# Optimization experiments

Measured on AMD Instinct MI355X. Metric: run time of the kernel, lower is better.

Reference implementation:

```python
import jax, jax.numpy as jnp
import numpy as np

NUM_BOND_TYPE = 6
NUM_BOND_DIRECTION = 3
N_NODES = 20000
N_EDGES = 320000
HIDDEN = 256
OUT = 256
N_MASK = 2000


def setup_inputs() -> dict:
    key = jax.random.key(0)
    ks = jax.random.split(key, 12)
    x = jax.random.normal(ks[0], (N_NODES, HIDDEN), dtype=jnp.float32)
    edge_index = jax.random.randint(ks[1], (2, N_EDGES), 0, N_NODES, dtype=jnp.int64)
    edge_attr = jax.random.randint(ks[2], (N_EDGES, 2), 0, 3, dtype=jnp.int64)
    mask_node_indices = jax.random.randint(ks[3], (N_MASK,), 0, N_NODES, dtype=jnp.int64)
    # parameters (torch Linear convention: y = x @ W.T + b)
    def xavier(k, shape):
        fan_in, fan_out = shape[1], shape[0]
        lim = float(np.sqrt(6.0 / (fan_in + fan_out)))
        return jax.random.uniform(k, shape, jnp.float32, -lim, lim)
    prelu_a = jnp.asarray(0.25, dtype=jnp.float32)  # torch PReLU default
    W_enc = xavier(ks[4], (HIDDEN, HIDDEN))          # enc_to_dec, no bias
    E1 = xavier(ks[5], (NUM_BOND_TYPE, HIDDEN))
    E2 = xavier(ks[6], (NUM_BOND_DIRECTION, HIDDEN))
    W1 = xavier(ks[7], (2 * HIDDEN, HIDDEN))
    b1 = jnp.zeros((2 * HIDDEN,), jnp.float32)
    W2 = xavier(ks[8], (OUT, 2 * HIDDEN))
    b2 = jnp.zeros((OUT,), jnp.float32)
    return {"x": x, "edge_index": edge_index, "edge_attr": edge_attr,
            "mask_node_indices": mask_node_indices, "prelu_a": prelu_a,
            "W_enc": W_enc, "E1": E1, "E2": E2,
            "W1": W1, "b1": b1, "W2": W2, "b2": b2}


def reference(x, edge_index, edge_attr, mask_node_indices, prelu_a,
              W_enc, E1, E2, W1, b1, W2, b2):
    N = x.shape[0]
    # PReLU -> enc_to_dec linear (no bias) -> zero masked rows
    x = jnp.where(x >= 0, x, prelu_a * x)
    x = x @ W_enc.T
    x = x.at[mask_node_indices].set(0.0)
    # add self loops: (i,i) edges with attr (4, 0)
    loop = jnp.arange(N, dtype=edge_index.dtype)
    ei = jnp.concatenate([edge_index, jnp.stack([loop, loop])], axis=1)  # [2, E+N]
    loop_attr = jnp.concatenate(
        [jnp.full((N, 1), 4, edge_attr.dtype), jnp.zeros((N, 1), edge_attr.dtype)], axis=1)
    ea = jnp.concatenate([edge_attr, loop_attr], axis=0)                 # [E+N, 2]
    edge_emb = E1[ea[:, 0]] + E2[ea[:, 1]]                               # [E+N, D]
    src, dst = ei[0], ei[1]                                              # j -> i
    msg = x[src] + edge_emb                                              # [E+N, D]
    aggr = jax.ops.segment_sum(msg, dst, num_segments=N)                 # [N, D]
    # GIN MLP: Linear -> ReLU -> Linear
    h = jax.nn.relu(aggr @ W1.T + b1)
    return h @ W2.T + b2
```

## Files before the change

### kernel.cpp

```cpp
#include <hip/hip_runtime.h>

#define HIDDEN 256
#define CAP 64

typedef _Float16 h4_t __attribute__((ext_vector_type(4)));
typedef _Float16 h8_t __attribute__((ext_vector_type(8)));
typedef float    f4_t __attribute__((ext_vector_type(4)));

typedef const __attribute__((address_space(1))) void* gbl_ptr_t;
typedef __attribute__((address_space(3))) void*       lds_ptr_t;

__device__ inline f4_t cvt4(h4_t h) {
    f4_t o; o.x = (float)h.x; o.y = (float)h.y; o.z = (float)h.z; o.w = (float)h.w;
    return o;
}

__global__ __launch_bounds__(256) void k_prep(
        const float* __restrict__ x, _Float16* __restrict__ xh,
        const float* __restrict__ prelu_a, int M, int Mpad, int nb_x,
        const int* __restrict__ ei, const int* __restrict__ ea, int E,
        int* __restrict__ cnt, int* __restrict__ csr, int nb_fill,
        const float* __restrict__ W_enc, const float* __restrict__ W1,
        const float* __restrict__ W2, _Float16* __restrict__ Whenc,
        _Float16* __restrict__ Wh1, _Float16* __restrict__ Wh2, int nb_w,
        const int* __restrict__ mask, unsigned char* __restrict__ flags, int NM) {
    int b = blockIdx.x;
    int t = threadIdx.x;
    if (b < nb_x) {
        int base = (b * 256 + t) * 4;
        if (base >= Mpad * HIDDEN) return;
        int row = base >> 8;
        h4_t o;
        if (row < M) {
            float pa = *prelu_a;
            f4_t v = *(const f4_t*)(x + base);
            o.x = (_Float16)(v.x >= 0.f ? v.x : pa * v.x);
            o.y = (_Float16)(v.y >= 0.f ? v.y : pa * v.y);
            o.z = (_Float16)(v.z >= 0.f ? v.z : pa * v.z);
            o.w = (_Float16)(v.w >= 0.f ? v.w : pa * v.w);
        } else {
            o = (h4_t)(_Float16)0.f;
        }
        *(h4_t*)(xh + base) = o;
        return;
    }
    b -= nb_x;
    if (b < nb_fill) {
        int e = b * 256 + t;
        if (e >= E) return;
        int src = ei[e];
        int dst = ei[E + e];
        int combo = ea[2 * e] * 3 + ea[2 * e + 1];
        int slot = atomicAdd(&cnt[dst], 1);
        if (slot < CAP) csr[dst * CAP + slot] = src | (combo << 16);
        return;
    }
    b -= nb_fill;
    if (b < nb_w) {
        const int n0 = HIDDEN * HIDDEN, n1 = 2 * HIDDEN * HIDDEN, n2 = HIDDEN * 2 * HIDDEN;
        int base = (b * 256 + t) * 4;
        const float* s; _Float16* d; int off;
        if (base < n0) { s = W_enc; d = Whenc; off = base; }
        else if (base < n0 + n1) { s = W1; d = Wh1; off = base - n0; }
        else if (base < n0 + n1 + n2) { s = W2; d = Wh2; off = base - n0 - n1; }
        else return;
        f4_t v = *(const f4_t*)(s + off);
        h4_t o; o.x = (_Float16)v.x; o.y = (_Float16)v.y;
        o.z = (_Float16)v.z; o.w = (_Float16)v.w;
        *(h4_t*)(d + off) = o;
        return;
    }
    b -= nb_w;
    {
        int i = b * 256 + t;
        if (i < NM) flags[mask[i]] = 1;
    }
}

__global__ __launch_bounds__(256) void k_aggregate(
        const _Float16* __restrict__ xe,
        const float* __restrict__ E1, const float* __restrict__ E2,
        const int* __restrict__ cnt, const int* __restrict__ csr,
        _Float16* __restrict__ aggr, int N, int Mpad) {
    __shared__ __align__(16) _Float16 e12h[18 * HIDDEN];
    int t = threadIdx.x;
    for (int idx = t; idx < 18 * 64; idx += 256) {
        int combo = idx >> 6, c4 = (idx & 63) * 4;
        int a1 = combo / 3, a2 = combo - a1 * 3;
        f4_t v1 = *(const f4_t*)(E1 + a1 * HIDDEN + c4);
        f4_t v2 = *(const f4_t*)(E2 + a2 * HIDDEN + c4);
        h4_t o;
        o.x = (_Float16)(v1.x + v2.x); o.y = (_Float16)(v1.y + v2.y);
        o.z = (_Float16)(v1.z + v2.z); o.w = (_Float16)(v1.w + v2.w);
        *(h4_t*)(e12h + combo * HIDDEN + c4) = o;
    }
    __syncthreads();
    int node = blockIdx.x * 4 + (t >> 6);
    if (node >= Mpad) return;
    int lane = t & 63;
    int c0 = lane * 4;
    if (node >= N) {
        *(h4_t*)(aggr + (size_t)node * HIDDEN + c0) = (h4_t)(_Float16)0.f;
        return;
    }
    int deg = cnt[node];
    if (deg > CAP) deg = CAP;
    const int* lst = csr + (size_t)node * CAP;
    int pv = (lane < deg) ? lst[lane] : 0;

    h4_t hs = *(const h4_t*)(xe + (size_t)node * HIDDEN + c0);
    h4_t se = *(const h4_t*)(e12h + 12 * HIDDEN + c0);
    f4_t acc = cvt4(hs) + cvt4(se);

    int e = 0;
    for (; e + 7 < deg; e += 8) {
        int p[8]; h4_t hv[8], qv[8];
#pragma unroll
        for (int j = 0; j < 8; ++j) p[j] = __shfl(pv, e + j, 64);
#pragma unroll
        for (int j = 0; j < 8; ++j)
            hv[j] = *(const h4_t*)(xe + (size_t)(p[j] & 0xFFFF) * HIDDEN + c0);
#pragma unroll
        for (int j = 0; j < 8; ++j)
            qv[j] = *(const h4_t*)(e12h + (p[j] >> 16) * HIDDEN + c0);
        h4_t s0 = (hv[0] + qv[0]) + (hv[1] + qv[1]);
        h4_t s1 = (hv[2] + qv[2]) + (hv[3] + qv[3]);
        h4_t s2 = (hv[4] + qv[4]) + (hv[5] + qv[5]);
        h4_t s3 = (hv[6] + qv[6]) + (hv[7] + qv[7]);
        acc += cvt4(s0) + cvt4(s1);
        acc += cvt4(s2) + cvt4(s3);
    }
    for (; e < deg; ++e) {
        int p = __shfl(pv, e, 64);
        h4_t h = *(const h4_t*)(xe + (size_t)(p & 0xFFFF) * HIDDEN + c0);
        h4_t q = *(const h4_t*)(e12h + (p >> 16) * HIDDEN + c0);
        acc += cvt4(h + q);
    }
    h4_t o;
    o.x = (_Float16)acc.x; o.y = (_Float16)acc.y;
    o.z = (_Float16)acc.z; o.w = (_Float16)acc.w;
    *(h4_t*)(aggr + (size_t)node * HIDDEN + c0) = o;
}

template <int K, bool RELU, bool HAS_BIAS, bool OUT_F16, bool MASK>
__global__ __launch_bounds__(256) void k_gemm128(
        const _Float16* __restrict__ A, const _Float16* __restrict__ B,
        const float* __restrict__ bias, void* __restrict__ Cout,
        const unsigned char* __restrict__ flags, int Mstore, int N) {
    __shared__ __align__(16) _Float16 As[128 * 32];
    __shared__ __align__(16) _Float16 Bs[128 * 32];
    int t = threadIdx.x;
    int w = t >> 6, L = t & 63;
    int wr = (w >> 1) * 64, wc = (w & 1) * 64;
    int m0 = blockIdx.y * 128, n0 = blockIdx.x * 128;
    int lr = L & 15, lk = (L >> 4) * 8;

    f4_t acc[4][4] = {};

    auto stage = [&](int k0) {
#pragma unroll
        for (int i = 0; i < 2; ++i) {
            int c = t + 256 * i;
            __builtin_amdgcn_global_load_lds(
                (gbl_ptr_t)(A + (size_t)(m0 + (c >> 2)) * K + k0 + (c & 3) * 8),
                (lds_ptr_t)(As + c * 8), 16, 0, 0);
        }
#pragma unroll
        for (int i = 0; i < 2; ++i) {
            int c = t + 256 * i;
            __builtin_amdgcn_global_load_lds(
                (gbl_ptr_t)(B + (size_t)(n0 + (c >> 2)) * K + k0 + (c & 3) * 8),
                (lds_ptr_t)(Bs + c * 8), 16, 0, 0);
        }
    };

    stage(0);
    constexpr int NS = K / 32;
#pragma unroll
    for (int s = 0; s < NS; ++s) {
        asm volatile("s_waitcnt vmcnt(0)" ::: "memory");
        __syncthreads();
        h8_t af[4], bf[4];
#pragma unroll
        for (int i = 0; i < 4; ++i) af[i] = *(const h8_t*)&As[(wr + i * 16 + lr) * 32 + lk];
#pragma unroll
        for (int j = 0; j < 4; ++j) bf[j] = *(const h8_t*)&Bs[(wc + j * 16 + lr) * 32 + lk];
        asm volatile("s_waitcnt lgkmcnt(0)" ::: "memory");
        __syncthreads();
        if (s + 1 < NS) stage((s + 1) * 32);
#pragma unroll
        for (int i = 0; i < 4; ++i)
#pragma unroll
            for (int j = 0; j < 4; ++j)
                acc[i][j] = __builtin_amdgcn_mfma_f32_16x16x32_f16(af[i], bf[j], acc[i][j], 0, 0, 0);
    }

    int lr4 = (L >> 4) * 4;
#pragma unroll
    for (int i = 0; i < 4; ++i)
#pragma unroll
        for (int r = 0; r < 4; ++r) {
            int row = m0 + wr + i * 16 + lr4 + r;
            float zm = 1.f;
            if constexpr (MASK) zm = flags[row] ? 0.f : 1.f;
#pragma unroll
            for (int j = 0; j < 4; ++j) {
                int col = n0 + wc + j * 16 + lr;
                float v = acc[i][j][r];
                if constexpr (HAS_BIAS) v += bias[col];
                if constexpr (RELU) v = v > 0.f ? v : 0.f;
                v *= zm;
                if constexpr (OUT_F16) {
                    ((_Float16*)Cout)[(size_t)row * N + col] = (_Float16)v;
                } else {
                    if (row < Mstore) ((float*)Cout)[(size_t)row * N + col] = v;
                }
            }
        }
}

extern "C" void kernel_launch(void* const* d_in, const int* in_sizes, int n_in,
                              void* d_out, int out_size, void* d_ws, size_t ws_size,
                              hipStream_t stream) {
    const float* x       = (const float*)d_in[0];
    const int*   ei      = (const int*)d_in[1];
    const int*   ea      = (const int*)d_in[2];
    const int*   mask    = (const int*)d_in[3];
    const float* prelu_a = (const float*)d_in[4];
    const float* W_enc   = (const float*)d_in[5];
    const float* E1      = (const float*)d_in[6];
    const float* E2      = (const float*)d_in[7];
    const float* W1      = (const float*)d_in[8];
    const float* b1      = (const float*)d_in[9];
    const float* W2      = (const float*)d_in[10];
    const float* b2      = (const float*)d_in[11];
    float*       out     = (float*)d_out;

    int N  = in_sizes[0] / HIDDEN;
    int E  = in_sizes[1] / 2;
    int NM = in_sizes[3];
    int Mpad = ((N + 127) / 128) * 128;

    char* ws = (char*)d_ws;
    size_t off = 0;
    _Float16* xh    = (_Float16*)(ws + off); off += (size_t)Mpad * HIDDEN * 2;
    _Float16* XEh   = (_Float16*)(ws + off); off += (size_t)Mpad * HIDDEN * 2;
    _Float16* AGh   = (_Float16*)(ws + off); off += (size_t)Mpad * HIDDEN * 2;
    _Float16* Hh    = (_Float16*)(ws + off); off += (size_t)Mpad * 2 * HIDDEN * 2;
    _Float16* Whenc = (_Float16*)(ws + off); off += (size_t)HIDDEN * HIDDEN * 2;
    _Float16* Wh1   = (_Float16*)(ws + off); off += (size_t)2 * HIDDEN * HIDDEN * 2;
    _Float16* Wh2   = (_Float16*)(ws + off); off += (size_t)HIDDEN * 2 * HIDDEN * 2;
    int* cnt        = (int*)(ws + off);      off += (size_t)N * 4;
    unsigned char* flags = (unsigned char*)(ws + off); off += (size_t)Mpad;
    off = (off + 15) & ~(size_t)15;
    int* csr        = (int*)(ws + off);      off += (size_t)N * CAP * 4;

    hipMemsetAsync(cnt, 0, (size_t)N * 4 + (size_t)Mpad, stream);

    int nb_x    = (Mpad * HIDDEN / 4 + 255) / 256;
    int nb_fill = (E + 255) / 256;
    int wtot4   = (HIDDEN * HIDDEN + 2 * HIDDEN * HIDDEN + HIDDEN * 2 * HIDDEN) / 4;
    int nb_w    = (wtot4 + 255) / 256;
    int nb_m    = (NM + 255) / 256;
    k_prep<<<nb_x + nb_fill + nb_w + nb_m, 256, 0, stream>>>(
        x, xh, prelu_a, N, Mpad, nb_x,
        ei, ea, E, cnt, csr, nb_fill,
        W_enc, W1, W2, Whenc, Wh1, Wh2, nb_w,
        mask, flags, NM);

    dim3 g1(HIDDEN / 128, Mpad / 128);
    k_gemm128<HIDDEN, false, false, true, true><<<g1, 256, 0, stream>>>(
        xh, Whenc, nullptr, XEh, flags, N, HIDDEN);

    k_aggregate<<<(Mpad + 3) / 4, 256, 0, stream>>>(XEh, E1, E2, cnt, csr, AGh, N, Mpad);

    dim3 g2(2 * HIDDEN / 128, Mpad / 128);
    k_gemm128<HIDDEN, true, true, true, false><<<g2, 256, 0, stream>>>(
        AGh, Wh1, b1, Hh, nullptr, N, 2 * HIDDEN);

    dim3 g3(HIDDEN / 128, Mpad / 128);
    k_gemm128<2 * HIDDEN, false, true, false, false><<<g3, 256, 0, stream>>>(
        Hh, Wh2, b2, out, nullptr, N, HIDDEN);
}
```

Measured before the change: 178.6 us.

## Fuse all stages into one cooperative persistent kernel with grid syncs

Replaces the memset plus five separate kernel launches with a single cooperative persistent kernel that performs prep, encoder GEMM, aggregation, and both MLP GEMMs, separated by grid-wide barriers. The GEMM body is factored into a shared device function, and the edge-embedding table is built per block in LDS. This removes launch gaps and the memset, at the cost of grid-sync overhead, a capped persistent grid that loops over tiles, and possibly lower occupancy from the combined kernel's register use. The multi-kernel path is kept as a fallback if the cooperative launch fails.

```diff
diff --git a/kernel.cpp b/kernel.cpp
--- a/kernel.cpp
+++ b/kernel.cpp
@@ -1,7 +1,10 @@
 #include <hip/hip_runtime.h>
+#include <hip/hip_cooperative_groups.h>
 
 #define HIDDEN 256
 #define CAP 64
+
+namespace cg = cooperative_groups;
 
 typedef _Float16 h4_t __attribute__((ext_vector_type(4)));
 typedef _Float16 h8_t __attribute__((ext_vector_type(8)));
@@ -13,6 +16,246 @@
 __device__ inline f4_t cvt4(h4_t h) {
     f4_t o; o.x = (float)h.x; o.y = (float)h.y; o.z = (float)h.z; o.w = (float)h.w;
     return o;
+}
+
+template <int K, bool RELU, bool HAS_BIAS, bool OUT_F16, bool MASK>
+__device__ __forceinline__ void gemm_tile(
+        _Float16* As, _Float16* Bs,
+        const _Float16* A, const _Float16* B,
+        const float* bias, void* Cout,
+        const unsigned char* flags, int Mstore, int N, int m0, int n0) {
+    int t = threadIdx.x;
+    int w = t >> 6, L = t & 63;
+    int wr = (w >> 1) * 64, wc = (w & 1) * 64;
+    int lr = L & 15, lk = (L >> 4) * 8;
+
+    f4_t acc[4][4] = {};
+
+    auto stage = [&](int k0) {
+#pragma unroll
+        for (int i = 0; i < 2; ++i) {
+            int c = t + 256 * i;
+            __builtin_amdgcn_global_load_lds(
+                (gbl_ptr_t)(A + (size_t)(m0 + (c >> 2)) * K + k0 + (c & 3) * 8),
+                (lds_ptr_t)(As + c * 8), 16, 0, 0);
+        }
+#pragma unroll
+        for (int i = 0; i < 2; ++i) {
+            int c = t + 256 * i;
+            __builtin_amdgcn_global_load_lds(
+                (gbl_ptr_t)(B + (size_t)(n0 + (c >> 2)) * K + k0 + (c & 3) * 8),
+                (lds_ptr_t)(Bs + c * 8), 16, 0, 0);
+        }
+    };
+
+    stage(0);
+    constexpr int NS = K / 32;
+#pragma unroll
+    for (int s = 0; s < NS; ++s) {
+        asm volatile("s_waitcnt vmcnt(0)" ::: "memory");
+        __syncthreads();
+        h8_t af[4], bf[4];
+#pragma unroll
+        for (int i = 0; i < 4; ++i) af[i] = *(const h8_t*)&As[(wr + i * 16 + lr) * 32 + lk];
+#pragma unroll
+        for (int j = 0; j < 4; ++j) bf[j] = *(const h8_t*)&Bs[(wc + j * 16 + lr) * 32 + lk];
+        asm volatile("s_waitcnt lgkmcnt(0)" ::: "memory");
+        __syncthreads();
+        if (s + 1 < NS) stage((s + 1) * 32);
+#pragma unroll
+        for (int i = 0; i < 4; ++i)
+#pragma unroll
+            for (int j = 0; j < 4; ++j)
+                acc[i][j] = __builtin_amdgcn_mfma_f32_16x16x32_f16(af[i], bf[j], acc[i][j], 0, 0, 0);
+    }
+
+    int lr4 = (L >> 4) * 4;
+#pragma unroll
+    for (int i = 0; i < 4; ++i)
+#pragma unroll
+        for (int r = 0; r < 4; ++r) {
+            int row = m0 + wr + i * 16 + lr4 + r;
+            float zm = 1.f;
+            if constexpr (MASK) zm = flags[row] ? 0.f : 1.f;
+#pragma unroll
+            for (int j = 0; j < 4; ++j) {
+                int col = n0 + wc + j * 16 + lr;
+                float v = acc[i][j][r];
+                if constexpr (HAS_BIAS) v += bias[col];
+                if constexpr (RELU) v = v > 0.f ? v : 0.f;
+                v *= zm;
+                if constexpr (OUT_F16) {
+                    ((_Float16*)Cout)[(size_t)row * N + col] = (_Float16)v;
+                } else {
+                    if (row < Mstore) ((float*)Cout)[(size_t)row * N + col] = v;
+                }
+            }
+        }
+}
+
+struct KP {
+    const float* x; const int* ei; const int* ea; const int* mask;
+    const float* prelu_a;
+    const float* W_enc; const float* E1; const float* E2;
+    const float* W1; const float* b1; const float* W2; const float* b2;
+    float* out;
+    _Float16 *xh, *XEh, *AGh, *Hh, *Whenc, *Wh1, *Wh2;
+    int* cnt; unsigned char* flags; int* csr;
+    int N, E, NM, Mpad;
+};
+
+__global__ __launch_bounds__(256, 3) void k_mega(KP p) {
+    __shared__ __align__(16) char smem[16384];
+    _Float16* As = (_Float16*)smem;
+    _Float16* Bs = (_Float16*)(smem + 8192);
+    cg::grid_group gg = cg::this_grid();
+    const int b = blockIdx.x, t = threadIdx.x, G = gridDim.x;
+
+    for (int i = b * 256 + t; i < p.N;    i += G * 256) p.cnt[i] = 0;
+    for (int i = b * 256 + t; i < p.Mpad; i += G * 256) p.flags[i] = 0;
+    gg.sync();
+
+    {
+        const int nb_x    = p.Mpad * (HIDDEN / 4) / 256;
+        const int nb_fill = (p.E + 255) / 256;
+        const int wtot4   = (HIDDEN*HIDDEN + 2*HIDDEN*HIDDEN + HIDDEN*2*HIDDEN) / 4;
+        const int nb_w    = (wtot4 + 255) / 256;
+        const int nb_m    = (p.NM + 255) / 256;
+        const int nbtot   = nb_x + nb_fill + nb_w + nb_m;
+        float pa = *p.prelu_a;
+        for (int u = b; u < nbtot; u += G) {
+            if (u < nb_x) {
+                int base = (u * 256 + t) * 4;
+                int row = base >> 8;
+                h4_t o;
+                if (row < p.N) {
+                    f4_t v = *(const f4_t*)(p.x + base);
+                    o.x = (_Float16)(v.x >= 0.f ? v.x : pa * v.x);
+                    o.y = (_Float16)(v.y >= 0.f ? v.y : pa * v.y);
+                    o.z = (_Float16)(v.z >= 0.f ? v.z : pa * v.z);
+                    o.w = (_Float16)(v.w >= 0.f ? v.w : pa * v.w);
+                } else {
+                    o = (h4_t)(_Float16)0.f;
+                }
+                *(h4_t*)(p.xh + base) = o;
+            } else if (u < nb_x + nb_fill) {
+                int e = (u - nb_x) * 256 + t;
+                if (e < p.E) {
+                    int src = p.ei[e];
+                    int dst = p.ei[p.E + e];
+                    int combo = p.ea[2 * e] * 3 + p.ea[2 * e + 1];
+                    int slot = atomicAdd(&p.cnt[dst], 1);
+                    if (slot < CAP) p.csr[dst * CAP + slot] = src | (combo << 16);
+                }
+            } else if (u < nb_x + nb_fill + nb_w) {
+                const int n0w = HIDDEN*HIDDEN, n1w = 2*HIDDEN*HIDDEN, n2w = HIDDEN*2*HIDDEN;
+                int base = ((u - nb_x - nb_fill) * 256 + t) * 4;
+                const float* s; _Float16* d; int off;
+                if (base < n0w)             { s = p.W_enc; d = p.Whenc; off = base; }
+                else if (base < n0w + n1w)  { s = p.W1;    d = p.Wh1;   off = base - n0w; }
+                else                        { s = p.W2;    d = p.Wh2;   off = base - n0w - n1w; }
+                f4_t v = *(const f4_t*)(s + off);
+                h4_t o; o.x = (_Float16)v.x; o.y = (_Float16)v.y;
+                o.z = (_Float16)v.z; o.w = (_Float16)v.w;
+                *(h4_t*)(d + off) = o;
+            } else {
+                int i = (u - nb_x - nb_fill - nb_w) * 256 + t;
+                if (i < p.NM) p.flags[p.mask[i]] = 1;
+            }
+        }
+    }
+    gg.sync();
+
+    {
+        const int nbx = HIDDEN / 128;
+        const int ntiles = nbx * (p.Mpad / 128);
+        for (int T = b; T < ntiles; T += G)
+            gemm_tile<HIDDEN, false, false, true, true>(
+                As, Bs, p.xh, p.Whenc, nullptr, p.XEh, p.flags, p.N, HIDDEN,
+                (T / nbx) * 128, (T % nbx) * 128);
+    }
+    gg.sync();
+
+    {
+        _Float16* e12h = (_Float16*)smem;
+        for (int idx = t; idx < 18 * 64; idx += 256) {
+            int combo = idx >> 6, c4 = (idx & 63) * 4;
+            int a1 = combo / 3, a2 = combo - a1 * 3;
+            f4_t v1 = *(const f4_t*)(p.E1 + a1 * HIDDEN + c4);
+            f4_t v2 = *(const f4_t*)(p.E2 + a2 * HIDDEN + c4);
+            h4_t o;
+            o.x = (_Float16)(v1.x + v2.x); o.y = (_Float16)(v1.y + v2.y);
+            o.z = (_Float16)(v1.z + v2.z); o.w = (_Float16)(v1.w + v2.w);
+            *(h4_t*)(e12h + combo * HIDDEN + c4) = o;
+        }
+        __syncthreads();
+        int w = t >> 6, lane = t & 63, c0 = lane * 4;
+        int ngr = p.Mpad / 4;
+        for (int g = b; g < ngr; g += G) {
+            int node = g * 4 + w;
+            if (node >= p.N) {
+                *(h4_t*)(p.AGh + (size_t)node * HIDDEN + c0) = (h4_t)(_Float16)0.f;
+                continue;
+            }
+            int deg = p.cnt[node];
+            if (deg > CAP) deg = CAP;
+            const int* lst = p.csr + (size_t)node * CAP;
+            int pv = (lane < deg) ? lst[lane] : 0;
+
+            h4_t hs = *(const h4_t*)(p.XEh + (size_t)node * HIDDEN + c0);
+            h4_t se = *(const h4_t*)(e12h + 12 * HIDDEN + c0);
+            f4_t acc = cvt4(hs) + cvt4(se);
+
+            int e = 0;
+            for (; e + 7 < deg; e += 8) {
+                int pp[8]; h4_t hv[8], qv[8];
+#pragma unroll
+                for (int j = 0; j < 8; ++j) pp[j] = __shfl(pv, e + j, 64);
+#pragma unroll
+                for (int j = 0; j < 8; ++j)
+                    hv[j] = *(const h4_t*)(p.XEh + (size_t)(pp[j] & 0xFFFF) * HIDDEN + c0);
+#pragma unroll
+                for (int j = 0; j < 8; ++j)
+                    qv[j] = *(const h4_t*)(e12h + (pp[j] >> 16) * HIDDEN + c0);
+                h4_t s0 = (hv[0] + qv[0]) + (hv[1] + qv[1]);
+                h4_t s1 = (hv[2] + qv[2]) + (hv[3] + qv[3]);
+                h4_t s2 = (hv[4] + qv[4]) + (hv[5] + qv[5]);
+                h4_t s3 = (hv[6] + qv[6]) + (hv[7] + qv[7]);
+                acc += cvt4(s0) + cvt4(s1);
+                acc += cvt4(s2) + cvt4(s3);
+            }
+            for (; e < deg; ++e) {
+                int pe = __shfl(pv, e, 64);
+                h4_t h = *(const h4_t*)(p.XEh + (size_t)(pe & 0xFFFF) * HIDDEN + c0);
+                h4_t q = *(const h4_t*)(e12h + (pe >> 16) * HIDDEN + c0);
+                acc += cvt4(h + q);
+            }
+            h4_t o;
+            o.x = (_Float16)acc.x; o.y = (_Float16)acc.y;
+            o.z = (_Float16)acc.z; o.w = (_Float16)acc.w;
+            *(h4_t*)(p.AGh + (size_t)node * HIDDEN + c0) = o;
+        }
+    }
+    gg.sync();
+
+    {
+        const int nbx = 2 * HIDDEN / 128;
+        const int ntiles = nbx * (p.Mpad / 128);
+        for (int T = b; T < ntiles; T += G)
+            gemm_tile<HIDDEN, true, true, true, false>(
+                As, Bs, p.AGh, p.Wh1, p.b1, p.Hh, nullptr, p.N, 2 * HIDDEN,
+                (T / nbx) * 128, (T % nbx) * 128);
+    }
+    gg.sync();
+
+    {
+        const int nbx = HIDDEN / 128;
+        const int ntiles = nbx * (p.Mpad / 128);
+        for (int T = b; T < ntiles; T += G)
+            gemm_tile<2 * HIDDEN, false, true, false, false>(
+                As, Bs, p.Hh, p.Wh2, p.b2, p.out, nullptr, p.N, HIDDEN,
+                (T / nbx) * 128, (T % nbx) * 128);
+    }
 }
 
 __global__ __launch_bounds__(256) void k_prep(
@@ -114,15 +357,15 @@
 
     int e = 0;
     for (; e + 7 < deg; e += 8) {
-        int p[8]; h4_t hv[8], qv[8];
-#pragma unroll
-        for (int j = 0; j < 8; ++j) p[j] = __shfl(pv, e + j, 64);
+        int pp[8]; h4_t hv[8], qv[8];
+#pragma unroll
+        for (int j = 0; j < 8; ++j) pp[j] = __shfl(pv, e + j, 64);
 #pragma unroll
         for (int j = 0; j < 8; ++j)
-            hv[j] = *(const h4_t*)(xe + (size_t)(p[j] & 0xFFFF) * HIDDEN + c0);
+            hv[j] = *(const h4_t*)(xe + (size_t)(pp[j] & 0xFFFF) * HIDDEN + c0);
 #pragma unroll
         for (int j = 0; j < 8; ++j)
-            qv[j] = *(const h4_t*)(e12h + (p[j] >> 16) * HIDDEN + c0);
+            qv[j] = *(const h4_t*)(e12h + (pp[j] >> 16) * HIDDEN + c0);
         h4_t s0 = (hv[0] + qv[0]) + (hv[1] + qv[1]);
         h4_t s1 = (hv[2] + qv[2]) + (hv[3] + qv[3]);
         h4_t s2 = (hv[4] + qv[4]) + (hv[5] + qv[5]);
@@ -131,9 +374,9 @@
         acc += cvt4(s2) + cvt4(s3);
     }
     for (; e < deg; ++e) {
-        int p = __shfl(pv, e, 64);
-        h4_t h = *(const h4_t*)(xe + (size_t)(p & 0xFFFF) * HIDDEN + c0);
-        h4_t q = *(const h4_t*)(e12h + (p >> 16) * HIDDEN + c0);
+        int pe = __shfl(pv, e, 64);
+        h4_t h = *(const h4_t*)(xe + (size_t)(pe & 0xFFFF) * HIDDEN + c0);
+        h4_t q = *(const h4_t*)(e12h + (pe >> 16) * HIDDEN + c0);
         acc += cvt4(h + q);
     }
     h4_t o;
@@ -147,76 +390,10 @@
         const _Float16* __restrict__ A, const _Float16* __restrict__ B,
         const float* __restrict__ bias, void* __restrict__ Cout,
         const unsigned char* __restrict__ flags, int Mstore, int N) {
-    __shared__ __align__(16) _Float16 As[128 * 32];
-    __shared__ __align__(16) _Float16 Bs[128 * 32];
-    int t = threadIdx.x;
-    int w = t >> 6, L = t & 63;
-    int wr = (w >> 1) * 64, wc = (w & 1) * 64;
-    int m0 = blockIdx.y * 128, n0 = blockIdx.x * 128;
-    int lr = L & 15, lk = (L >> 4) * 8;
-
-    f4_t acc[4][4] = {};
-
-    auto stage = [&](int k0) {
-#pragma unroll
-        for (int i = 0; i < 2; ++i) {
-            int c = t + 256 * i;
-            __builtin_amdgcn_global_load_lds(
-                (gbl_ptr_t)(A + (size_t)(m0 + (c >> 2)) * K + k0 + (c & 3) * 8),
-                (lds_ptr_t)(As + c * 8), 16, 0, 0);
-        }
-#pragma unroll
-        for (int i = 0; i < 2; ++i) {
-            int c = t + 256 * i;
-            __builtin_amdgcn_global_load_lds(
-                (gbl_ptr_t)(B + (size_t)(n0 + (c >> 2)) * K + k0 + (c & 3) * 8),
-                (lds_ptr_t)(Bs + c * 8), 16, 0, 0);
-        }
-    };
-
-    stage(0);
-    constexpr int NS = K / 32;
-#pragma unroll
-    for (int s = 0; s < NS; ++s) {
-        asm volatile("s_waitcnt vmcnt(0)" ::: "memory");
-        __syncthreads();
-        h8_t af[4], bf[4];
-#pragma unroll
-        for (int i = 0; i < 4; ++i) af[i] = *(const h8_t*)&As[(wr + i * 16 + lr) * 32 + lk];
-#pragma unroll
-        for (int j = 0; j < 4; ++j) bf[j] = *(const h8_t*)&Bs[(wc + j * 16 + lr) * 32 + lk];
-        asm volatile("s_waitcnt lgkmcnt(0)" ::: "memory");
-        __syncthreads();
-        if (s + 1 < NS) stage((s + 1) * 32);
-#pragma unroll
-        for (int i = 0; i < 4; ++i)
-#pragma unroll
-            for (int j = 0; j < 4; ++j)
-                acc[i][j] = __builtin_amdgcn_mfma_f32_16x16x32_f16(af[i], bf[j], acc[i][j], 0, 0, 0);
-    }
-
-    int lr4 = (L >> 4) * 4;
-#pragma unroll
-    for (int i = 0; i < 4; ++i)
-#pragma unroll
-        for (int r = 0; r < 4; ++r) {
-            int row = m0 + wr + i * 16 + lr4 + r;
-            float zm = 1.f;
-            if constexpr (MASK) zm = flags[row] ? 0.f : 1.f;
-#pragma unroll
-            for (int j = 0; j < 4; ++j) {
-                int col = n0 + wc + j * 16 + lr;
-                float v = acc[i][j][r];
-                if constexpr (HAS_BIAS) v += bias[col];
-                if constexpr (RELU) v = v > 0.f ? v : 0.f;
-                v *= zm;
-                if constexpr (OUT_F16) {
-                    ((_Float16*)Cout)[(size_t)row * N + col] = (_Float16)v;
-                } else {
-                    if (row < Mstore) ((float*)Cout)[(size_t)row * N + col] = v;
-                }
-            }
-        }
+    __shared__ __align__(16) char smem[16384];
+    gemm_tile<K, RELU, HAS_BIAS, OUT_F16, MASK>(
+        (_Float16*)smem, (_Float16*)(smem + 8192),
+        A, B, bias, Cout, flags, Mstore, N, blockIdx.y * 128, blockIdx.x * 128);
 }
 
 extern "C" void kernel_launch(void* const* d_in, const int* in_sizes, int n_in,
@@ -255,30 +432,39 @@
     off = (off + 15) & ~(size_t)15;
     int* csr        = (int*)(ws + off);      off += (size_t)N * CAP * 4;
 
-    hipMemsetAsync(cnt, 0, (size_t)N * 4 + (size_t)Mpad, stream);
-
-    int nb_x    = (Mpad * HIDDEN / 4 + 255) / 256;
-    int nb_fill = (E + 255) / 256;
-    int wtot4   = (HIDDEN * HIDDEN + 2 * HIDDEN * HIDDEN + HIDDEN * 2 * HIDDEN) / 4;
-    int nb_w    = (wtot4 + 255) / 256;
-    int nb_m    = (NM + 255) / 256;
-    k_prep<<<nb_x + nb_fill + nb_w + nb_m, 256, 0, stream>>>(
-        x, xh, prelu_a, N, Mpad, nb_x,
-        ei, ea, E, cnt, csr, nb_fill,
-        W_enc, W1, W2, Whenc, Wh1, Wh2, nb_w,
-        mask, flags, NM);
-
-    dim3 g1(HIDDEN / 128, Mpad / 128);
-    k_gemm128<HIDDEN, false, false, true, true><<<g1, 256, 0, stream>>>(
-        xh, Whenc, nullptr, XEh, flags, N, HIDDEN);
-
-    k_aggregate<<<(Mpad + 3) / 4, 256, 0, stream>>>(XEh, E1, E2, cnt, csr, AGh, N, Mpad);
-
-    dim3 g2(2 * HIDDEN / 128, Mpad / 128);
-    k_gemm128<HIDDEN, true, true, true, false><<<g2, 256, 0, stream>>>(
-        AGh, Wh1, b1, Hh, nullptr, N, 2 * HIDDEN);
-
-    dim3 g3(HIDDEN / 128, Mpad / 128);
-    k_gemm128<2 * HIDDEN, false, true, false, false><<<g3, 256, 0, stream>>>(
-        Hh, Wh2, b2, out, nullptr, N, HIDDEN);
-}
+    KP kp{x, ei, ea, mask, prelu_a, W_enc, E1, E2, W1, b1, W2, b2, out,
+          xh, XEh, AGh, Hh, Whenc, Wh1, Wh2, cnt, flags, csr, N, E, NM, Mpad};
+
+    int mb = 0;
+    hipError_t qerr = hipOccupancyMaxActiveBlocksPerMultiprocessor(&mb, k_mega, 256, 0);
+    if (qerr != hipSuccess || mb < 1) mb = 1;
+    int grid = mb * 256;
+    if (grid > 2048) grid = 2048;
+    void* args[] = { &kp };
+    hipError_t cerr = hipLaunchCooperativeKernel(
+        (const void*)k_mega, dim3(grid), dim3(256), args, 0, stream);
+
+    if (cerr != hipSuccess) {
+        hipMemsetAsync(cnt, 0, (size_t)N * 4 + (size_t)Mpad, stream);
+        int nb_x    = (Mpad * HIDDEN / 4 + 255) / 256;
+        int nb_fill = (E + 255) / 256;
+        int wtot4   = (HIDDEN * HIDDEN + 2 * HIDDEN * HIDDEN + HIDDEN * 2 * HIDDEN) / 4;
+        int nb_w    = (wtot4 + 255) / 256;
+        int nb_m    = (NM + 255) / 256;
+        k_prep<<<nb_x + nb_fill + nb_w + nb_m, 256, 0, stream>>>(
+            x, xh, prelu_a, N, Mpad, nb_x,
+            ei, ea, E, cnt, csr, nb_fill,
+            W_enc, W1, W2, Whenc, Wh1, Wh2, nb_w,
+            mask, flags, NM);
+        dim3 g1(HIDDEN / 128, Mpad / 128);
+        k_gemm128<HIDDEN, false, false, true, true><<<g1, 256, 0, stream>>>(
+            xh, Whenc, nullptr, XEh, flags, N, HIDDEN);
+        k_aggregate<<<(Mpad + 3) / 4, 256, 0, stream>>>(XEh, E1, E2, cnt, csr, AGh, N, Mpad);
+        dim3 g2(2 * HIDDEN / 128, Mpad / 128);
+        k_gemm128<HIDDEN, true, true, true, false><<<g2, 256, 0, stream>>>(
+            AGh, Wh1, b1, Hh, nullptr, N, 2 * HIDDEN);
+        dim3 g3(HIDDEN / 128, Mpad / 128);
+        k_gemm128<2 * HIDDEN, false, true, false, false><<<g3, 256, 0, stream>>>(
+            Hh, Wh2, b2, out, nullptr, N, HIDDEN);
+    }
+}
```

Result: slower. 415.2 us (+132.4%).
